# Kernel tuning notes

Hardware: AMD Instinct MI355X
Metric: run time of the kernel (lower is better)

Reference implementation:

```python
import jax, jax.numpy as jnp
import numpy as np

B, T, L = 64, 256, 64          # batch, time steps, num_links
H = 128                        # hidden_size
E = 524288                     # num edges
N = B * T                      # nodes seen by GCNConv
IN = L + L * L                 # 4160: concat of link features + flattened distance matrix
OUT = 12 * L                   # fc output size
NUM_LSTM = 2


def setup_inputs() -> dict:
    key = jax.random.key(0)
    ks = jax.random.split(key, 24)
    inp = {
        "x": jax.random.normal(ks[0], (B, T, L), jnp.float32),
        "distance": jax.random.uniform(ks[1], (L, L), jnp.float32),
        "edge_index": jax.random.randint(ks[2], (2, E), 0, N, jnp.int64),
    }
    # GCN layer params (PyG GCNConv: lin weight [in,out] acting as x @ W, bias after aggregation)
    dims = [IN, H, H, H]
    for i in range(3):
        s = 1.0 / np.sqrt(dims[i])
        inp[f"gcn_W{i}"] = jax.random.normal(ks[3 + 2 * i], (dims[i], H), jnp.float32) * s
        inp[f"gcn_b{i}"] = jnp.zeros((H,), jnp.float32)
    # LSTM params, torch layout: W_ih [4H, Hin], W_hh [4H, H], gate order i,f,g,o
    s = 1.0 / np.sqrt(H)
    for l in range(NUM_LSTM):
        inp[f"Wih{l}"] = jax.random.normal(ks[10 + 4 * l], (4 * H, H), jnp.float32) * s
        inp[f"Whh{l}"] = jax.random.normal(ks[11 + 4 * l], (4 * H, H), jnp.float32) * s
        inp[f"bih{l}"] = jax.random.normal(ks[12 + 4 * l], (4 * H,), jnp.float32) * s
        inp[f"bhh{l}"] = jax.random.normal(ks[13 + 4 * l], (4 * H,), jnp.float32) * s
    inp["fc_W"] = jax.random.normal(ks[20], (OUT, H), jnp.float32) * s
    inp["fc_b"] = jnp.zeros((OUT,), jnp.float32)
    return inp


def _gcn(x, W, b, src, dst):
    # GCNConv with add_self_loops=True: out = D^-1/2 (A+I) D^-1/2 (x W) + b
    h = x @ W
    deg = jnp.ones((N,), h.dtype).at[dst].add(1.0)  # in-degree + self loop
    dinv = jax.lax.rsqrt(deg)
    norm = dinv[src] * dinv[dst]                    # [E]
    agg = jnp.zeros_like(h).at[dst].add(h[src] * norm[:, None])
    agg = agg + h * (dinv * dinv)[:, None]          # self-loop term
    return agg + b


def _lstm_layer(xs, Wih, Whh, bih, bhh):
    # xs: [T, B, Hin]
    bias = bih + bhh

    def step(carry, xt):
        h, c = carry
        g = xt @ Wih.T + h @ Whh.T + bias
        i, f, gg, o = jnp.split(g, 4, axis=-1)
        c = jax.nn.sigmoid(f) * c + jax.nn.sigmoid(i) * jnp.tanh(gg)
        h = jax.nn.sigmoid(o) * jnp.tanh(c)
        return (h, c), h

    h0 = jnp.zeros((xs.shape[1], H), xs.dtype)
    _, ys = jax.lax.scan(step, (h0, h0), xs)
    return ys


def reference(x, distance, gcn_W0, gcn_b0, gcn_W1, gcn_b1, gcn_W2, gcn_b2,
              Wih0, Whh0, bih0, bhh0, Wih1, Whh1, bih1, bhh1, fc_W, fc_b,
              edge_index):
    src, dst = edge_index[0], edge_index[1]
    xf = x.reshape(N, L)
    dist_flat = jnp.broadcast_to(distance.reshape(1, L * L), (N, L * L))
    feat = jnp.concatenate([xf, dist_flat], axis=1)  # [N, IN]
    for W, b in ((gcn_W0, gcn_b0), (gcn_W1, gcn_b1), (gcn_W2, gcn_b2)):
        feat = jax.nn.relu(_gcn(feat, W, b, src, dst))
    seq = feat.reshape(B, T, H).transpose(1, 0, 2)   # [T, B, H]
    seq = _lstm_layer(seq, Wih0, Whh0, bih0, bhh0)
    seq = _lstm_layer(seq, Wih1, Whh1, bih1, bhh1)
    last = seq[-1]                                   # [B, H]
    out = last @ fc_W.T + fc_b                       # [B, OUT]
    return out.reshape(B, 12, L)
```

## Files before the change

### kernel.cpp

```cpp
#include <hip/hip_runtime.h>
#include <hip/hip_bf16.h>
#include <cstdint>
#include <cstddef>

#define NB 64
#define NT 256
#define NL 64
#define NH 128
#define NN 16384
#define NE 524288
#define NG 512
#define NOUT 768


__global__ __launch_bounds__(256) void k_transpose(const float* __restrict__ W,
                                                   float* __restrict__ Wt,
                                                   int K, int Nout) {
  int i = blockIdx.x * 256 + threadIdx.x;
  if (i < K * Nout) {
    int k = i / Nout, n = i % Nout;
    Wt[n * K + k] = W[i];
  }
}

__global__ __launch_bounds__(256) void k_dvec(const float* __restrict__ dist,
                                              const float* __restrict__ W0,
                                              float* __restrict__ dvec) {
  __shared__ float red[256];
  int j = blockIdx.x;
  int t = threadIdx.x;
  float acc = 0.f;
  for (int m = t; m < 4096; m += 256)
    acc += dist[m] * W0[(size_t)(64 + m) * 128 + j];
  red[t] = acc;
  __syncthreads();
  for (int off = 128; off > 0; off >>= 1) {
    if (t < off) red[t] += red[t + off];
    __syncthreads();
  }
  if (t == 0) dvec[j] = red[0];
}

__global__ __launch_bounds__(256) void k_count(const int* __restrict__ dst,
                                               int* __restrict__ counts) {
  int i = blockIdx.x * 256 + threadIdx.x;
  atomicAdd(&counts[dst[i]], 1);
}

__global__ __launch_bounds__(256) void k_dinv(const int* __restrict__ counts,
                                              float* __restrict__ dinv) {
  int n = blockIdx.x * 256 + threadIdx.x;
  dinv[n] = rsqrtf((float)counts[n] + 1.0f);
}

__global__ __launch_bounds__(1024) void k_scan(const int* __restrict__ counts,
                                               int* __restrict__ rowstart) {
  __shared__ int part[1024];
  int t = threadIdx.x;
  int base = t * 16;
  int local[16];
  int s = 0;
#pragma unroll
  for (int i = 0; i < 16; i++) { local[i] = s; s += counts[base + i]; }
  part[t] = s;
  __syncthreads();
  for (int off = 1; off < 1024; off <<= 1) {
    int v = (t >= off) ? part[t - off] : 0;
    __syncthreads();
    part[t] += v;
    __syncthreads();
  }
  int prefix = (t == 0) ? 0 : part[t - 1];
#pragma unroll
  for (int i = 0; i < 16; i++) rowstart[base + i] = prefix + local[i];
  if (t == 1023) rowstart[16384] = part[1023];
}

__global__ __launch_bounds__(256) void k_fill(const int* __restrict__ src,
                                              const int* __restrict__ dst,
                                              const int* __restrict__ rowstart,
                                              int* __restrict__ fill,
                                              const float* __restrict__ dinv,
                                              int2* __restrict__ csr) {
  int e = blockIdx.x * 256 + threadIdx.x;
  int sN = src[e], dN = dst[e];
  int pos = rowstart[dN] + atomicAdd(&fill[dN], 1);
  csr[pos] = make_int2(sN, __float_as_int(dinv[sN] * dinv[dN]));
}

template <int K, bool RELU, bool PERMC = false>
__global__ __launch_bounds__(256) void k_gemm_abt(const float* __restrict__ A,
                                                  const float* __restrict__ Bm,
                                                  const float* __restrict__ bias0,
                                                  const float* __restrict__ bias1,
                                                  float* __restrict__ C, int Nn) {
  __shared__ float As[64][K + 1];
  __shared__ float Bs[64][K + 1];
  const int tid = threadIdx.x;
  const int bm = blockIdx.x, bn = blockIdx.y;
  const int VPR = K / 4;
  for (int i = tid; i < 64 * VPR; i += 256) {
    int r = i / VPR, v = (i % VPR) * 4;
    float4 q = *(const float4*)(A + (size_t)(bm * 64 + r) * K + v);
    As[r][v] = q.x; As[r][v + 1] = q.y; As[r][v + 2] = q.z; As[r][v + 3] = q.w;
  }
  for (int i = tid; i < 64 * VPR; i += 256) {
    int r = i / VPR, v = (i % VPR) * 4;
    float4 q = *(const float4*)(Bm + (size_t)(bn * 64 + r) * K + v);
    Bs[r][v] = q.x; Bs[r][v + 1] = q.y; Bs[r][v + 2] = q.z; Bs[r][v + 3] = q.w;
  }
  __syncthreads();
  const int tr = (tid >> 4) << 2;
  const int tc = (tid & 15) << 2;
  float acc[4][4] = {};
#pragma unroll 4
  for (int k = 0; k < K; k++) {
    float a0 = As[tr + 0][k], a1 = As[tr + 1][k], a2 = As[tr + 2][k], a3 = As[tr + 3][k];
    float b0 = Bs[tc + 0][k], b1 = Bs[tc + 1][k], b2 = Bs[tc + 2][k], b3 = Bs[tc + 3][k];
    acc[0][0] += a0 * b0; acc[0][1] += a0 * b1; acc[0][2] += a0 * b2; acc[0][3] += a0 * b3;
    acc[1][0] += a1 * b0; acc[1][1] += a1 * b1; acc[1][2] += a1 * b2; acc[1][3] += a1 * b3;
    acc[2][0] += a2 * b0; acc[2][1] += a2 * b1; acc[2][2] += a2 * b2; acc[2][3] += a2 * b3;
    acc[3][0] += a3 * b0; acc[3][1] += a3 * b1; acc[3][2] += a3 * b2; acc[3][3] += a3 * b3;
  }
#pragma unroll
  for (int i2 = 0; i2 < 4; i2++) {
    int row = bm * 64 + tr + i2;
#pragma unroll
    for (int j2 = 0; j2 < 4; j2++) {
      int col = bn * 64 + tc + j2;
      float v = acc[i2][j2];
      if (bias0) v += bias0[col];
      if (bias1) v += bias1[col];
      if (RELU) v = fmaxf(v, 0.f);
      int colw = PERMC ? ((col & 127) * 4 + (col >> 7)) : col;
      C[(size_t)row * Nn + colw] = v;
    }
  }
}

__global__ __launch_bounds__(256) void k_agg(const float* __restrict__ h,
                                             const int* __restrict__ rowstart,
                                             const int2* __restrict__ csr,
                                             const float* __restrict__ dinv,
                                             const float* __restrict__ bias,
                                             float* __restrict__ out) {
  int node = blockIdx.x * 4 + (threadIdx.x >> 6);
  int lane = threadIdx.x & 63;
  int s = rowstart[node], e = rowstart[node + 1];
  const float2* h2 = (const float2*)h;
  float ax = 0.f, ay = 0.f;
  int p = s;
  for (; p + 1 < e; p += 2) {
    int2 pk0 = csr[p];
    int2 pk1 = csr[p + 1];
    float2 hv0 = h2[(size_t)pk0.x * 64 + lane];
    float2 hv1 = h2[(size_t)pk1.x * 64 + lane];
    float w0 = __int_as_float(pk0.y);
    float w1 = __int_as_float(pk1.y);
    ax = fmaf(hv0.x, w0, ax); ay = fmaf(hv0.y, w0, ay);
    ax = fmaf(hv1.x, w1, ax); ay = fmaf(hv1.y, w1, ay);
  }
  if (p < e) {
    int2 pk0 = csr[p];
    float2 hv0 = h2[(size_t)pk0.x * 64 + lane];
    float w0 = __int_as_float(pk0.y);
    ax = fmaf(hv0.x, w0, ax); ay = fmaf(hv0.y, w0, ay);
  }
  float di = dinv[node];
  float sw = di * di;
  float2 hs = h2[(size_t)node * 64 + lane];
  float2 bv = ((const float2*)bias)[lane];
  ax = fmaf(hs.x, sw, ax) + bv.x;
  ay = fmaf(hs.y, sw, ay) + bv.y;
  float2 o;
  o.x = fmaxf(ax, 0.f);
  o.y = fmaxf(ay, 0.f);
  ((float2*)out)[(size_t)node * 64 + lane] = o;
}


template <int CTRL>
__device__ __forceinline__ float dppadd(float x) {
  int r = __builtin_amdgcn_update_dpp(0, __float_as_int(x), CTRL, 0xF, 0xF, true);
  return x + __int_as_float(r);
}

__device__ __forceinline__ float sigf(float x) {
  return 1.f / (1.f + __expf(-x));
}
__device__ __forceinline__ float tanhf_fast(float x) {
  return 1.f - 2.f / (__expf(2.f * x) + 1.f);
}

typedef float f4v __attribute__((ext_vector_type(4)));

template <bool LAST_ONLY>
__global__ __launch_bounds__(512)
__attribute__((amdgpu_waves_per_eu(2, 2)))
void k_lstm7(const float* __restrict__ pre,
             const float* __restrict__ Whh,
             float* __restrict__ yout) {
  __shared__ float hbuf[2][128];
  const int tid = threadIdx.x;
  const int b = blockIdx.x;
  const int c4 = tid & 3;
  const int u = tid >> 2;

  int hidx[8];
#pragma unroll
  for (int j = 0; j < 8; j++) hidx[j] = c4 * 8 + (((u & 7) + 2 * c4 + j) & 7);

#define DECLW(g, j) \
  f4v W##g##_##j = *(const f4v*)(Whh + (size_t)((g)*128 + u) * 128 + hidx[j] * 4);
#define DECLW_ROW(g) \
  DECLW(g, 0) DECLW(g, 1) DECLW(g, 2) DECLW(g, 3) \
  DECLW(g, 4) DECLW(g, 5) DECLW(g, 6) DECLW(g, 7)
  DECLW_ROW(0) DECLW_ROW(1) DECLW_ROW(2) DECLW_ROW(3)
#undef DECLW_ROW
#undef DECLW

  if (tid < 128) hbuf[0][tid] = 0.f;
  float cs = 0.f;
  const float* preb = pre + (size_t)b * NT * NG + tid;
  float pcur = preb[0];
  float* ybase = LAST_ONLY ? (yout + (size_t)b * NH + u)
                           : (yout + (size_t)b * NT * NH + u);
  __syncthreads();

#define PINW(g) \
  asm volatile("" : "+v"(W##g##_0), "+v"(W##g##_1), "+v"(W##g##_2), "+v"(W##g##_3)); \
  asm volatile("" : "+v"(W##g##_4), "+v"(W##g##_5), "+v"(W##g##_6), "+v"(W##g##_7));

#define FMA_J(j)                                                               \
  {                                                                            \
    f4v hv = hp[hidx[j]];                                                      \
    a0 = __builtin_elementwise_fma(W0_##j, hv, a0);                            \
    a1 = __builtin_elementwise_fma(W1_##j, hv, a1);                            \
    a2 = __builtin_elementwise_fma(W2_##j, hv, a2);                            \
    a3 = __builtin_elementwise_fma(W3_##j, hv, a3);                            \
  }

#define LSTM_STEP(CUR, NXT, T)                                                 \
  {                                                                            \
    int tn = (T) + 1; if (tn > NT - 1) tn = NT - 1;                            \
    float pnext = preb[(size_t)tn * NG];                                       \
    const f4v* hp = (const f4v*)&hbuf[CUR][0];                                 \
    f4v a0 = {0.f, 0.f, 0.f, 0.f}, a1 = a0, a2 = a0, a3 = a0;                  \
    FMA_J(0) FMA_J(1) FMA_J(2) FMA_J(3)                                        \
    FMA_J(4) FMA_J(5) FMA_J(6) FMA_J(7)                                        \
    float s0 = (a0.x + a0.y) + (a0.z + a0.w) + ((c4 == 0) ? pcur : 0.f);       \
    float s1 = (a1.x + a1.y) + (a1.z + a1.w) + ((c4 == 1) ? pcur : 0.f);       \
    float s2 = (a2.x + a2.y) + (a2.z + a2.w) + ((c4 == 2) ? pcur : 0.f);       \
    float s3 = (a3.x + a3.y) + (a3.z + a3.w) + ((c4 == 3) ? pcur : 0.f);       \
    s0 = dppadd<0xB1>(s0); s0 = dppadd<0x4E>(s0);                              \
    s1 = dppadd<0xB1>(s1); s1 = dppadd<0x4E>(s1);                              \
    s2 = dppadd<0xB1>(s2); s2 = dppadd<0x4E>(s2);                              \
    s3 = dppadd<0xB1>(s3); s3 = dppadd<0x4E>(s3);                              \
    float si = sigf(s0), sf = sigf(s1), tg = tanhf_fast(s2), so = sigf(s3);    \
    cs = sf * cs + si * tg;                                                    \
    float hnew = so * tanhf_fast(cs);                                          \
    if (c4 == 0) hbuf[NXT][u] = hnew;                                          \
    if (!LAST_ONLY) {                                                          \
      if (c4 == 1) ybase[(size_t)(T) * NH] = hnew;                             \
    } else if ((T) == NT - 1) {                                                \
      if (c4 == 1) *ybase = hnew;                                              \
    }                                                                          \
    pcur = pnext;                                                              \
    __syncthreads();                                                           \
  }

  for (int t = 0; t < NT; t += 2) {
    PINW(0) PINW(1) PINW(2) PINW(3)
    LSTM_STEP(0, 1, t);
    LSTM_STEP(1, 0, t + 1);
  }
#undef LSTM_STEP
#undef FMA_J
#undef PINW
}


extern "C" void kernel_launch(void* const* d_in, const int* in_sizes, int n_in,
                              void* d_out, int out_size, void* d_ws, size_t ws_size,
                              hipStream_t stream) {
  const float* x    = (const float*)d_in[0];
  const float* dist = (const float*)d_in[1];
  const int*   ei   = (const int*)d_in[2];
  const float* W0   = (const float*)d_in[3];
  const float* b0   = (const float*)d_in[4];
  const float* W1   = (const float*)d_in[5];
  const float* b1   = (const float*)d_in[6];
  const float* W2   = (const float*)d_in[7];
  const float* b2   = (const float*)d_in[8];
  const float* Wih0 = (const float*)d_in[9];
  const float* Whh0 = (const float*)d_in[10];
  const float* bih0 = (const float*)d_in[11];
  const float* bhh0 = (const float*)d_in[12];
  const float* Wih1 = (const float*)d_in[13];
  const float* Whh1 = (const float*)d_in[14];
  const float* bih1 = (const float*)d_in[15];
  const float* bhh1 = (const float*)d_in[16];
  const float* fcW  = (const float*)d_in[17];
  const float* fcb  = (const float*)d_in[18];
  float* out = (float*)d_out;

  char* ws = (char*)d_ws;
  size_t off = 0;
  auto alloc = [&](size_t bytes) -> void* {
    void* p = ws + off;
    off += (bytes + 255) & ~(size_t)255;
    return p;
  };
  float* bufA     = (float*)alloc((size_t)NN * 128 * 4);
  float* bufB     = (float*)alloc((size_t)NN * 128 * 4);
  float* pre      = (float*)alloc((size_t)NN * 512 * 4);
  int2*  csr      = (int2*)alloc((size_t)NE * 8);
  int*   counts   = (int*)alloc((size_t)NN * 4);
  int*   fillc    = (int*)alloc((size_t)NN * 4);
  int*   rowstart = (int*)alloc((size_t)(NN + 1) * 4);
  float* dinv     = (float*)alloc((size_t)NN * 4);
  float* dvec     = (float*)alloc(128 * 4);
  float* hlast    = (float*)alloc(64 * 128 * 4);
  float* wt0      = (float*)alloc(128 * 64 * 4);
  float* wt1      = (float*)alloc(128 * 128 * 4);
  float* wt2      = (float*)alloc(128 * 128 * 4);
  (void)ws_size; (void)in_sizes; (void)n_in; (void)out_size;

  const int* srcIdx = ei;
  const int* dstIdx = ei + NE;

  hipMemsetAsync(counts, 0, (size_t)NN * 4, stream);
  hipMemsetAsync(fillc, 0, (size_t)NN * 4, stream);

  k_transpose<<<(64 * 128 + 255) / 256, 256, 0, stream>>>(W0, wt0, 64, 128);
  k_transpose<<<(128 * 128 + 255) / 256, 256, 0, stream>>>(W1, wt1, 128, 128);
  k_transpose<<<(128 * 128 + 255) / 256, 256, 0, stream>>>(W2, wt2, 128, 128);
  k_dvec<<<128, 256, 0, stream>>>(dist, W0, dvec);

  k_count<<<NE / 256, 256, 0, stream>>>(dstIdx, counts);
  k_scan<<<1, 1024, 0, stream>>>(counts, rowstart);
  k_dinv<<<NN / 256, 256, 0, stream>>>(counts, dinv);
  k_fill<<<NE / 256, 256, 0, stream>>>(srcIdx, dstIdx, rowstart, fillc, dinv, csr);

  dim3 gH(NN / 64, 128 / 64);
  k_gemm_abt<64, false><<<gH, 256, 0, stream>>>(x, wt0, dvec, nullptr, bufB, 128);
  k_agg<<<NN / 4, 256, 0, stream>>>(bufB, rowstart, csr, dinv, b0, bufA);
  k_gemm_abt<128, false><<<gH, 256, 0, stream>>>(bufA, wt1, nullptr, nullptr, bufB, 128);
  k_agg<<<NN / 4, 256, 0, stream>>>(bufB, rowstart, csr, dinv, b1, bufA);
  k_gemm_abt<128, false><<<gH, 256, 0, stream>>>(bufA, wt2, nullptr, nullptr, bufB, 128);
  k_agg<<<NN / 4, 256, 0, stream>>>(bufB, rowstart, csr, dinv, b2, bufA);

  dim3 gP(NN / 64, 512 / 64);
  k_gemm_abt<128, false, true><<<gP, 256, 0, stream>>>(bufA, Wih0, bih0, bhh0, pre, 512);
  k_lstm7<false><<<64, 512, 0, stream>>>(pre, Whh0, bufB);
  k_gemm_abt<128, false, true><<<gP, 256, 0, stream>>>(bufB, Wih1, bih1, bhh1, pre, 512);
  k_lstm7<true><<<64, 512, 0, stream>>>(pre, Whh1, hlast);

  dim3 gF(1, NOUT / 64);
  k_gemm_abt<128, false><<<gF, 256, 0, stream>>>(hlast, fcW, fcb, nullptr, out, NOUT);
}
```

Baseline: 888.0 us.

## Pack LSTM recurrent weights to bf16 and reload from cache each step

Adds a pre-pass that converts each recurrent weight matrix to bf16, packed in a per-thread interleaved layout. The LSTM kernel then reloads these weights from global memory (expected to hit L1/L2) at every time step instead of keeping 128 fp32 values pinned in registers. This lowers register pressure and may allow better scheduling, at the cost of 16 vector loads per step on the serial critical path and reduced weight precision.

```diff
diff --git a/kernel.cpp b/kernel.cpp
--- a/kernel.cpp
+++ b/kernel.cpp
@@ -86,6 +86,30 @@
   int sN = src[e], dN = dst[e];
   int pos = rowstart[dN] + atomicAdd(&fill[dN], 1);
   csr[pos] = make_int2(sN, __float_as_int(dinv[sN] * dinv[dN]));
+}
+
+__device__ __forceinline__ unsigned rne_bf16(float f) {
+  unsigned u = __float_as_uint(f);
+  return (u + 0x7FFFu + ((u >> 16) & 1u)) >> 16;
+}
+
+__global__ __launch_bounds__(256) void k_packw(const float* __restrict__ Whh,
+                                               uint4* __restrict__ out) {
+  int idx = blockIdx.x * 256 + threadIdx.x;
+  int c = idx >> 9, tid = idx & 511;
+  int u = tid >> 2, c4 = tid & 3;
+  int g = c >> 2, q = c & 3;
+  int h0 = c4 * 8 + (((u & 7) + 2 * c4 + 2 * q) & 7);
+  int h1 = c4 * 8 + (((u & 7) + 2 * c4 + 2 * q + 1) & 7);
+  const float* row = Whh + (size_t)(g * 128 + u) * 128;
+  const float* p0 = row + h0 * 4;
+  const float* p1 = row + h1 * 4;
+  uint4 o;
+  o.x = rne_bf16(p0[0]) | (rne_bf16(p0[1]) << 16);
+  o.y = rne_bf16(p0[2]) | (rne_bf16(p0[3]) << 16);
+  o.z = rne_bf16(p1[0]) | (rne_bf16(p1[1]) << 16);
+  o.w = rne_bf16(p1[2]) | (rne_bf16(p1[3]) << 16);
+  out[c * 512 + tid] = o;
 }
 
 template <int K, bool RELU, bool PERMC = false>
@@ -192,13 +216,24 @@
   return 1.f - 2.f / (__expf(2.f * x) + 1.f);
 }
 
+typedef float f2v __attribute__((ext_vector_type(2)));
 typedef float f4v __attribute__((ext_vector_type(4)));
+
+__device__ __forceinline__ f2v unpk(unsigned d) {
+  f2v r;
+  r.x = __uint_as_float(d << 16);
+  r.y = __uint_as_float(d & 0xFFFF0000u);
+  return r;
+}
+__device__ __forceinline__ f2v mk2(float a, float b) {
+  f2v r; r.x = a; r.y = b; return r;
+}
 
 template <bool LAST_ONLY>
 __global__ __launch_bounds__(512)
 __attribute__((amdgpu_waves_per_eu(2, 2)))
-void k_lstm7(const float* __restrict__ pre,
-             const float* __restrict__ Whh,
+void k_lstm8(const float* __restrict__ pre,
+             const uint4* __restrict__ wpk,
              float* __restrict__ yout) {
   __shared__ float hbuf[2][128];
   const int tid = threadIdx.x;
@@ -209,15 +244,6 @@
   int hidx[8];
 #pragma unroll
   for (int j = 0; j < 8; j++) hidx[j] = c4 * 8 + (((u & 7) + 2 * c4 + j) & 7);
-
-#define DECLW(g, j) \
-  f4v W##g##_##j = *(const f4v*)(Whh + (size_t)((g)*128 + u) * 128 + hidx[j] * 4);
-#define DECLW_ROW(g) \
-  DECLW(g, 0) DECLW(g, 1) DECLW(g, 2) DECLW(g, 3) \
-  DECLW(g, 4) DECLW(g, 5) DECLW(g, 6) DECLW(g, 7)
-  DECLW_ROW(0) DECLW_ROW(1) DECLW_ROW(2) DECLW_ROW(3)
-#undef DECLW_ROW
-#undef DECLW
 
   if (tid < 128) hbuf[0][tid] = 0.f;
   float cs = 0.f;
@@ -227,31 +253,38 @@
                            : (yout + (size_t)b * NT * NH + u);
   __syncthreads();
 
-#define PINW(g) \
-  asm volatile("" : "+v"(W##g##_0), "+v"(W##g##_1), "+v"(W##g##_2), "+v"(W##g##_3)); \
-  asm volatile("" : "+v"(W##g##_4), "+v"(W##g##_5), "+v"(W##g##_6), "+v"(W##g##_7));
-
-#define FMA_J(j)                                                               \
+#define GATE(g, SG)                                                            \
   {                                                                            \
-    f4v hv = hp[hidx[j]];                                                      \
-    a0 = __builtin_elementwise_fma(W0_##j, hv, a0);                            \
-    a1 = __builtin_elementwise_fma(W1_##j, hv, a1);                            \
-    a2 = __builtin_elementwise_fma(W2_##j, hv, a2);                            \
-    a3 = __builtin_elementwise_fma(W3_##j, hv, a3);                            \
+    f2v ag = {0.f, 0.f};                                                       \
+    _Pragma("unroll")                                                          \
+    for (int q = 0; q < 4; q++) {                                              \
+      uint4 wd = wv[(g) * 4 + q];                                              \
+      f4v ha = hp[hidx[2 * q]];                                                \
+      f4v hb = hp[hidx[2 * q + 1]];                                            \
+      ag = __builtin_elementwise_fma(unpk(wd.x), mk2(ha.x, ha.y), ag);         \
+      ag = __builtin_elementwise_fma(unpk(wd.y), mk2(ha.z, ha.w), ag);         \
+      ag = __builtin_elementwise_fma(unpk(wd.z), mk2(hb.x, hb.y), ag);         \
+      ag = __builtin_elementwise_fma(unpk(wd.w), mk2(hb.z, hb.w), ag);         \
+    }                                                                          \
+    SG = ag.x + ag.y;                                                          \
   }
 
 #define LSTM_STEP(CUR, NXT, T)                                                 \
   {                                                                            \
     int tn = (T) + 1; if (tn > NT - 1) tn = NT - 1;                            \
     float pnext = preb[(size_t)tn * NG];                                       \
+    const uint4* wq = wpk;                                                     \
+    asm volatile("" : "+s"(wq));   \
+    uint4 wv[16];                                                              \
+    _Pragma("unroll")                                                          \
+    for (int c = 0; c < 16; c++) wv[c] = wq[c * 512 + tid];                    \
     const f4v* hp = (const f4v*)&hbuf[CUR][0];                                 \
-    f4v a0 = {0.f, 0.f, 0.f, 0.f}, a1 = a0, a2 = a0, a3 = a0;                  \
-    FMA_J(0) FMA_J(1) FMA_J(2) FMA_J(3)                                        \
-    FMA_J(4) FMA_J(5) FMA_J(6) FMA_J(7)                                        \
-    float s0 = (a0.x + a0.y) + (a0.z + a0.w) + ((c4 == 0) ? pcur : 0.f);       \
-    float s1 = (a1.x + a1.y) + (a1.z + a1.w) + ((c4 == 1) ? pcur : 0.f);       \
-    float s2 = (a2.x + a2.y) + (a2.z + a2.w) + ((c4 == 2) ? pcur : 0.f);       \
-    float s3 = (a3.x + a3.y) + (a3.z + a3.w) + ((c4 == 3) ? pcur : 0.f);       \
+    float s0, s1, s2, s3;                                                      \
+    GATE(0, s0) GATE(1, s1) GATE(2, s2) GATE(3, s3)                            \
+    s0 += (c4 == 0) ? pcur : 0.f;                                              \
+    s1 += (c4 == 1) ? pcur : 0.f;                                              \
+    s2 += (c4 == 2) ? pcur : 0.f;                                              \
+    s3 += (c4 == 3) ? pcur : 0.f;                                              \
     s0 = dppadd<0xB1>(s0); s0 = dppadd<0x4E>(s0);                              \
     s1 = dppadd<0xB1>(s1); s1 = dppadd<0x4E>(s1);                              \
     s2 = dppadd<0xB1>(s2); s2 = dppadd<0x4E>(s2);                              \
@@ -270,13 +303,11 @@
   }
 
   for (int t = 0; t < NT; t += 2) {
-    PINW(0) PINW(1) PINW(2) PINW(3)
     LSTM_STEP(0, 1, t);
     LSTM_STEP(1, 0, t + 1);
   }
 #undef LSTM_STEP
-#undef FMA_J
-#undef PINW
+#undef GATE
 }
 
 
@@ -324,6 +355,8 @@
   float* wt0      = (float*)alloc(128 * 64 * 4);
   float* wt1      = (float*)alloc(128 * 128 * 4);
   float* wt2      = (float*)alloc(128 * 128 * 4);
+  uint4* wpk0     = (uint4*)alloc((size_t)8192 * 16);
+  uint4* wpk1     = (uint4*)alloc((size_t)8192 * 16);
   (void)ws_size; (void)in_sizes; (void)n_in; (void)out_size;
 
   const int* srcIdx = ei;
@@ -336,6 +369,8 @@
   k_transpose<<<(128 * 128 + 255) / 256, 256, 0, stream>>>(W1, wt1, 128, 128);
   k_transpose<<<(128 * 128 + 255) / 256, 256, 0, stream>>>(W2, wt2, 128, 128);
   k_dvec<<<128, 256, 0, stream>>>(dist, W0, dvec);
+  k_packw<<<32, 256, 0, stream>>>(Whh0, wpk0);
+  k_packw<<<32, 256, 0, stream>>>(Whh1, wpk1);
 
   k_count<<<NE / 256, 256, 0, stream>>>(dstIdx, counts);
   k_scan<<<1, 1024, 0, stream>>>(counts, rowstart);
@@ -352,9 +387,9 @@
 
   dim3 gP(NN / 64, 512 / 64);
   k_gemm_abt<128, false, true><<<gP, 256, 0, stream>>>(bufA, Wih0, bih0, bhh0, pre, 512);
-  k_lstm7<false><<<64, 512, 0, stream>>>(pre, Whh0, bufB);
+  k_lstm8<false><<<64, 512, 0, stream>>>(pre, wpk0, bufB);
   k_gemm_abt<128, false, true><<<gP, 256, 0, stream>>>(bufB, Wih1, bih1, bhh1, pre, 512);
-  k_lstm7<true><<<64, 512, 0, stream>>>(pre, Whh1, hlast);
+  k_lstm8<true><<<64, 512, 0, stream>>>(pre, wpk1, hlast);
 
   dim3 gF(1, NOUT / 64);
   k_gemm_abt<128, false><<<gF, 256, 0, stream>>>(hlast, fcW, fcb, nullptr, out, NOUT);
```

Result: slower. 1.471 ms (+65.6%).
